# Performance work log

Hardware: AMD Instinct MI355X
Metric: run time of the kernel (lower is better)

## Reference

```python
import jax, jax.numpy as jnp
import numpy as np

BLK = 128          # quantization block size (group_shape = (1,128) act, (128,128) weight)
FP8_MAX = 448.0    # max finite value of float8_e4m3fn
EPS = 1e-6         # RMSNorm epsilon


def _rms_norm(x, weight):
    # RMSNorm: x / sqrt(mean(x^2) + eps) * weight
    var = jnp.mean(x * x, axis=-1, keepdims=True)
    return x * jax.lax.rsqrt(var + EPS) * weight


def _quant_dequant_act(x):
    # Per-token-group (1, BLK) dynamic FP8 quantization, then dequant (fake-quant).
    M, K = x.shape
    g = x.reshape(M, K // BLK, BLK)
    scale = jnp.maximum(jnp.max(jnp.abs(g), axis=-1, keepdims=True) / FP8_MAX, 1e-10)
    q = jnp.clip(g / scale, -FP8_MAX, FP8_MAX)
    q = q.astype(jnp.float8_e4m3fn).astype(jnp.float32)
    return (q * scale).reshape(M, K)


def _dequant_weight(w_fp8, ws):
    # w_fp8: [N, K] fp8-rounded values in fp32; ws: [N//BLK, K//BLK] block scales.
    s_full = jnp.repeat(jnp.repeat(ws, BLK, axis=0), BLK, axis=1)  # [N, K]
    return w_fp8 * s_full


def setup_inputs() -> dict:
    key = jax.random.key(0)
    k1, k2, k3, k4 = jax.random.split(key, 4)
    T, H = 4096, 4096
    x = jax.random.normal(k1, (T, H), dtype=jnp.float32)
    norm_w = jax.random.uniform(k2, (4, H), dtype=jnp.float32)
    w = jax.random.uniform(k3, (3, H, H), dtype=jnp.float32)
    wscale = jax.random.uniform(k4, (3, H // BLK, H // BLK), dtype=jnp.float32)
    return {"x": x, "norm_w": norm_w, "w": w, "wscale": wscale}


def reference(x, norm_w, w, wscale):
    # Weights are stored as FP8 in the original model (torch.rand(...).to(FP8_DTYPE)).
    w_fp8 = w.astype(jnp.float8_e4m3fn).astype(jnp.float32)  # [3, H, H]

    x = jax.nn.relu(x)
    resid = x
    # norm[0]: plain RMSNorm
    y = _rms_norm(x, norm_w[0])
    for i in range(3):
        # block-FP8 linear: quantize activation, dequantize weight, out = a @ W^T
        a = _quant_dequant_act(y)                    # [T, H]
        wd = _dequant_weight(w_fp8[i], wscale[i])    # [H, H]
        xi = a @ wd.T                                # [T, H]
        # fused add + RMSNorm: resid = xi + resid; y = rmsnorm(resid)
        resid = xi + resid
        y = _rms_norm(resid, norm_w[i + 1])
    return y
```

## Files before the change

### kernel.cpp

```cpp
#include <hip/hip_runtime.h>

typedef float f32x4 __attribute__((ext_vector_type(4)));
typedef long lx2 __attribute__((ext_vector_type(2)));

#define HDIM 4096
#define NKB 32

__device__ __forceinline__ int frag_off(int off) {
  const int o = off & 127;
  return (off & ~127) + (o & 64) + ((o & 24) << 1) + ((o & 32) >> 2) + (o & 7);
}

__global__ __launch_bounds__(256) void wquant_kernel(const float* __restrict__ w,
                                                     unsigned char* __restrict__ w8,
                                                     int n4) {
  int i = blockIdx.x * 256 + threadIdx.x;
  if (i >= n4) return;
  const float4 v = ((const float4*)w)[i];
  int p = 0;
  p = __builtin_amdgcn_cvt_pk_fp8_f32(v.x, v.y, p, false);
  p = __builtin_amdgcn_cvt_pk_fp8_f32(v.z, v.w, p, true);
  const int row = i >> 10;
  const int off = (i << 2) & 4095;
  *(int*)(w8 + (size_t)row * HDIM + frag_off(off)) = p;
}

template <int MODE>
__global__ __launch_bounds__(256) void norm_quant_kernel(
    const float* __restrict__ src, float* __restrict__ resid,
    const float* __restrict__ nw, unsigned char* __restrict__ qa,
    float* __restrict__ ascT, float* __restrict__ out) {
  const int row = blockIdx.x;
  const int tid = threadIdx.x;
  const float* srow = src + (size_t)row * HDIM;
  float4 v[4];
  float ss = 0.f;
#pragma unroll
  for (int c = 0; c < 4; ++c) {
    float4 t = ((const float4*)srow)[c * 256 + tid];
    if (MODE == 0) {
      t.x = fmaxf(t.x, 0.f); t.y = fmaxf(t.y, 0.f);
      t.z = fmaxf(t.z, 0.f); t.w = fmaxf(t.w, 0.f);
      ((float4*)(resid + (size_t)row * HDIM))[c * 256 + tid] = t;
    }
    v[c] = t;
    ss += t.x * t.x + t.y * t.y + t.z * t.z + t.w * t.w;
  }
#pragma unroll
  for (int m = 32; m >= 1; m >>= 1) ss += __shfl_xor(ss, m);
  __shared__ float red[4];
  if ((tid & 63) == 0) red[tid >> 6] = ss;
  __syncthreads();
  const float tot = red[0] + red[1] + red[2] + red[3];
  const float rstd = rsqrtf(tot * (1.f / (float)HDIM) + 1e-6f);
#pragma unroll
  for (int c = 0; c < 4; ++c) {
    float4 wv = ((const float4*)nw)[c * 256 + tid];
    float4 y;
    y.x = v[c].x * rstd * wv.x;
    y.y = v[c].y * rstd * wv.y;
    y.z = v[c].z * rstd * wv.z;
    y.w = v[c].w * rstd * wv.w;
    if (MODE == 2) {
      ((float4*)(out + (size_t)row * HDIM))[c * 256 + tid] = y;
    } else {
      float amax = fmaxf(fmaxf(fabsf(y.x), fabsf(y.y)), fmaxf(fabsf(y.z), fabsf(y.w)));
#pragma unroll
      for (int m = 16; m >= 1; m >>= 1) amax = fmaxf(amax, __shfl_xor(amax, m));
      const float scale = fmaxf(amax / 448.f, 1e-10f);
      const float qinv = __builtin_amdgcn_rcpf(scale);
      float qx = fminf(fmaxf(y.x * qinv, -448.f), 448.f);
      float qy = fminf(fmaxf(y.y * qinv, -448.f), 448.f);
      float qz = fminf(fmaxf(y.z * qinv, -448.f), 448.f);
      float qw = fminf(fmaxf(y.w * qinv, -448.f), 448.f);
      int p = 0;
      p = __builtin_amdgcn_cvt_pk_fp8_f32(qx, qy, p, false);
      p = __builtin_amdgcn_cvt_pk_fp8_f32(qz, qw, p, true);
      const int off = (c * 256 + tid) << 2;
      *(int*)(qa + (size_t)row * HDIM + frag_off(off)) = p;
      if ((tid & 31) == 0) ascT[(c * 8 + (tid >> 5)) * HDIM + row] = scale;
    }
  }
}

__device__ __forceinline__ f32x4 chain4(const lx2 (&a)[2], const lx2 (&b)[2]) {
  f32x4 t = __builtin_amdgcn_mfma_f32_16x16x32_fp8_fp8(a[0].x, b[0].x,
                                                       (f32x4){0.f, 0.f, 0.f, 0.f}, 0, 0, 0);
  t = __builtin_amdgcn_mfma_f32_16x16x32_fp8_fp8(a[0].y, b[0].y, t, 0, 0, 0);
  t = __builtin_amdgcn_mfma_f32_16x16x32_fp8_fp8(a[1].x, b[1].x, t, 0, 0, 0);
  t = __builtin_amdgcn_mfma_f32_16x16x32_fp8_fp8(a[1].y, b[1].y, t, 0, 0, 0);
  return t;
}

__global__ __launch_bounds__(512, 2) void gemm256_kernel(
    const unsigned char* __restrict__ qa, const float* __restrict__ ascT,
    const unsigned char* __restrict__ w8, const float* __restrict__ wsc,
    float* __restrict__ resid) {
  extern __shared__ char smem[];
  char* ldsA = smem;
  char* ldsB = smem + 65536;
  char* ldsS = smem + 131072;

  const int tid = threadIdx.x;
  const int lane = tid & 63;
  const int wid = tid >> 6;
  const int wm = wid >> 1;
  const int wn = wid & 1;

  const int bflat = blockIdx.y * 16 + blockIdx.x;
  const int bswz = (bflat & 7) * 32 + (bflat >> 3);
  const int m0 = (bswz >> 4) << 8;
  const int n0 = (bswz & 15) << 8;

  const int ln15 = lane & 15;
  const int g = lane >> 4;

  int ofsA[4], ofsB[4];
  {
    const int mt_ = (tid >> 7) & 3, kh_ = (tid >> 6) & 1;
    const int col = kh_ * 64 + ((tid >> 4) & 3) * 16;
    const int rr_ = tid & 15;
#pragma unroll
    for (int ch = 0; ch < 4; ++ch) {
      ofsA[ch] = (ch * 64 + mt_ * 16 + rr_) * HDIM + col;
      ofsB[ch] = ((ch >> 1) * 128 + ((ch & 1) * 4 + mt_) * 16 + rr_) * HDIM + col;
    }
  }
  const unsigned char* gA = qa + (size_t)m0 * HDIM;
  const unsigned char* gB = w8 + (size_t)n0 * HDIM;
  const float* sS = ascT + m0 + lane * 4;

  const int nb = __builtin_amdgcn_readfirstlane((n0 >> 7) + wn);
  const float* wsp = wsc + nb * NKB;

  const int abase = wm * 8192 + lane * 16;
  const int bbase = wn * 16384 + lane * 16;
  const int svb = wm * 256 + g * 16;

  f32x4 acc[4][8];
#pragma unroll
  for (int i = 0; i < 4; ++i)
#pragma unroll
    for (int j = 0; j < 8; ++j) acc[i][j] = (f32x4){0.f, 0.f, 0.f, 0.f};

  lx2 aF[4][2];
  lx2 bFa[2][2];
  lx2 bFb[2][2];
  f32x4 svw[4];

#define STAGE_A(CH, KB, BUF)                                                              \
  __builtin_amdgcn_global_load_lds(                                                       \
      (const __attribute__((address_space(1))) void*)(gA + ofsA[CH] + (KB)*128),          \
      (__attribute__((address_space(3))) void*)(ldsA + (BUF)*32768 + (CH)*8192 + tid*16), \
      16, 0, 0)
#define STAGE_B(CH, KB, BUF)                                                              \
  __builtin_amdgcn_global_load_lds(                                                       \
      (const __attribute__((address_space(1))) void*)(gB + ofsB[CH] + (KB)*128),          \
      (__attribute__((address_space(3))) void*)(ldsB + (BUF)*32768 + (CH)*8192 + tid*16), \
      16, 0, 0)
#define STAGE_S(KB, BUF)                                                                  \
  __builtin_amdgcn_global_load_lds(                                                       \
      (const __attribute__((address_space(1))) void*)(sS + (size_t)(KB)*HDIM),            \
      (__attribute__((address_space(3))) void*)(ldsS + (BUF)*1024 + lane*16), 16, 0, 0)

#define RD_A(MT)                                                                          \
  aF[MT][0] = *(const lx2*)(ldsA + cb + abase + (MT)*2048);                               \
  aF[MT][1] = *(const lx2*)(ldsA + cb + abase + (MT)*2048 + 1024);
#define RD_SVW(MT) svw[MT] = *(const f32x4*)(ldsS + cur * 1024 + svb + (MT)*64) * sw;
#define RD_BS(BS, NH)                                                                     \
  BS[0][0] = *(const lx2*)(ldsB + cb + bbase + ((NH)*2) * 2048);                          \
  BS[0][1] = *(const lx2*)(ldsB + cb + bbase + ((NH)*2) * 2048 + 1024);                   \
  BS[1][0] = *(const lx2*)(ldsB + cb + bbase + ((NH)*2 + 1) * 2048);                      \
  BS[1][1] = *(const lx2*)(ldsB + cb + bbase + ((NH)*2 + 1) * 2048 + 1024);

#define PH_SYNC                                                                           \
  __builtin_amdgcn_s_barrier();                                                           \
  asm volatile("s_waitcnt lgkmcnt(0)" ::: "memory");                                      \
  __builtin_amdgcn_sched_barrier(0);

#define MFMA_PH(MTA, MTB, NH, BS)                                                         \
  __builtin_amdgcn_s_setprio(1);                                                          \
  {                                                                                       \
    f32x4 t0 = chain4(aF[MTA], BS[0]);                                                    \
    f32x4 t1 = chain4(aF[MTA], BS[1]);                                                    \
    f32x4 t2 = chain4(aF[MTB], BS[0]);                                                    \
    f32x4 t3 = chain4(aF[MTB], BS[1]);                                                    \
    __builtin_amdgcn_s_setprio(0);                                                        \
    acc[MTA][(NH)*2]     += t0 * svw[MTA];                                                \
    acc[MTA][(NH)*2 + 1] += t1 * svw[MTA];                                                \
    acc[MTB][(NH)*2]     += t2 * svw[MTB];                                                \
    acc[MTB][(NH)*2 + 1] += t3 * svw[MTB];                                                \
  }

  STAGE_S(0, 0); STAGE_A(0, 0, 0); STAGE_A(1, 0, 0); STAGE_A(2, 0, 0); STAGE_A(3, 0, 0);
  STAGE_B(0, 0, 0); STAGE_B(2, 0, 0); STAGE_B(1, 0, 0); STAGE_B(3, 0, 0);
  asm volatile("s_waitcnt vmcnt(2)" ::: "memory");
  __builtin_amdgcn_s_barrier();

#pragma unroll 2
  for (int kb = 0; kb < NKB; ++kb) {
    const int cur = kb & 1;
    const int nxt = cur ^ 1;
    const int kbn = (kb + 1) & (NKB - 1);
    const int cb = cur * 32768;
    const float sw = wsp[kb];
    RD_A(0) RD_A(1) RD_SVW(0) RD_SVW(1) RD_BS(bFa, 0)
    STAGE_S(kbn, nxt); STAGE_A(0, kbn, nxt);
    PH_SYNC MFMA_PH(0, 1, 0, bFa)
    __builtin_amdgcn_s_barrier();
    RD_A(2) RD_A(3) RD_SVW(2) RD_SVW(3)
    STAGE_A(1, kbn, nxt); STAGE_A(2, kbn, nxt);
    PH_SYNC MFMA_PH(2, 3, 0, bFa)
    __builtin_amdgcn_s_barrier();
    RD_BS(bFb, 1)
    STAGE_A(3, kbn, nxt); STAGE_B(0, kbn, nxt);
    PH_SYNC MFMA_PH(2, 3, 1, bFb)
    __builtin_amdgcn_s_barrier();
    PH_SYNC MFMA_PH(0, 1, 1, bFb)
    asm volatile("s_waitcnt vmcnt(6)" ::: "memory");
    __builtin_amdgcn_s_barrier();
    RD_BS(bFa, 2)
    STAGE_B(2, kbn, nxt);
    PH_SYNC MFMA_PH(0, 1, 2, bFa)
    __builtin_amdgcn_s_barrier();
    STAGE_B(1, kbn, nxt);
    PH_SYNC MFMA_PH(2, 3, 2, bFa)
    __builtin_amdgcn_s_barrier();
    RD_BS(bFb, 3)
    STAGE_B(3, kbn, nxt);
    PH_SYNC MFMA_PH(2, 3, 3, bFb)
    __builtin_amdgcn_s_barrier();
    PH_SYNC MFMA_PH(0, 1, 3, bFb)
    asm volatile("s_waitcnt vmcnt(2)" ::: "memory");
    __builtin_amdgcn_s_barrier();
  }

  const size_t rowstart = (size_t)(m0 + wm * 64 + g * 4) * HDIM + n0 + wn * 128 + ln15;
#pragma unroll
  for (int mt = 0; mt < 4; ++mt)
#pragma unroll
    for (int ntg = 0; ntg < 8; ++ntg)
#pragma unroll
      for (int j = 0; j < 4; ++j) {
        const size_t idx = rowstart + (size_t)(mt * 16 + j) * HDIM + ntg * 16;
        resid[idx] += acc[mt][ntg][j];
      }
#undef MFMA_PH
#undef PH_SYNC
#undef RD_BS
#undef RD_SVW
#undef RD_A
#undef STAGE_A
#undef STAGE_B
#undef STAGE_S
}

extern "C" void kernel_launch(void* const* d_in, const int* in_sizes, int n_in,
                              void* d_out, int out_size, void* d_ws, size_t ws_size,
                              hipStream_t stream) {
  const float* x = (const float*)d_in[0];
  const float* norm_w = (const float*)d_in[1];
  const float* w = (const float*)d_in[2];
  const float* wscale = (const float*)d_in[3];
  float* out = (float*)d_out;
  char* ws = (char*)d_ws;

  size_t off = 0;
  unsigned char* w8 = (unsigned char*)(ws + off); off += 3ull * HDIM * HDIM;
  float* resid = (float*)(ws + off);              off += (size_t)HDIM * HDIM * 4;
  unsigned char* qa = (unsigned char*)(ws + off); off += (size_t)HDIM * HDIM;
  float* asc = (float*)(ws + off);                off += (size_t)NKB * HDIM * 4;

  hipFuncSetAttribute((const void*)gemm256_kernel,
                      hipFuncAttributeMaxDynamicSharedMemorySize, 133120);

  const int n4 = 3 * HDIM * HDIM / 4;
  wquant_kernel<<<n4 / 256, 256, 0, stream>>>(w, w8, n4);
  norm_quant_kernel<0><<<HDIM, 256, 0, stream>>>(x, resid, norm_w, qa, asc, nullptr);
  for (int i = 0; i < 3; ++i) {
    gemm256_kernel<<<dim3(16, 16), 512, 133120, stream>>>(
        qa, asc, w8 + (size_t)i * HDIM * HDIM, wscale + i * NKB * NKB, resid);
    if (i < 2)
      norm_quant_kernel<1><<<HDIM, 256, 0, stream>>>(resid, nullptr, norm_w + (size_t)(i + 1) * HDIM, qa, asc, nullptr);
    else
      norm_quant_kernel<2><<<HDIM, 256, 0, stream>>>(resid, nullptr, norm_w + (size_t)3 * HDIM, nullptr, nullptr, out);
  }
}
```

Measured before the change: 478.6 us.

## Use 16x16x128 scaled FP8 MFMA and drop fragment-permuted layouts

Replaces each chain of four 16x16x32 FP8 MFMAs with a single gfx950 mfma_scale 16x16x128 f8f6f4 instruction using a neutral scale of 127. Because that instruction takes contiguous 32-byte K fragments, the quantization kernels now store FP8 activations and weights in plain row-major order instead of a permuted fragment layout, and the GEMM staging offsets are unified. The aim is fewer, denser matrix instructions and simpler quant stores. The risk is that the new K-ordering in LDS must match the operand layout the wider instruction expects, otherwise results would be wrong.

```diff
diff --git a/kernel.cpp b/kernel.cpp
--- a/kernel.cpp
+++ b/kernel.cpp
@@ -1,15 +1,11 @@
 #include <hip/hip_runtime.h>
 
 typedef float f32x4 __attribute__((ext_vector_type(4)));
-typedef long lx2 __attribute__((ext_vector_type(2)));
+typedef int i32x4 __attribute__((ext_vector_type(4)));
+typedef int i32x8 __attribute__((ext_vector_type(8)));
 
 #define HDIM 4096
 #define NKB 32
-
-__device__ __forceinline__ int frag_off(int off) {
-  const int o = off & 127;
-  return (off & ~127) + (o & 64) + ((o & 24) << 1) + ((o & 32) >> 2) + (o & 7);
-}
 
 __global__ __launch_bounds__(256) void wquant_kernel(const float* __restrict__ w,
                                                      unsigned char* __restrict__ w8,
@@ -20,9 +16,7 @@
   int p = 0;
   p = __builtin_amdgcn_cvt_pk_fp8_f32(v.x, v.y, p, false);
   p = __builtin_amdgcn_cvt_pk_fp8_f32(v.z, v.w, p, true);
-  const int row = i >> 10;
-  const int off = (i << 2) & 4095;
-  *(int*)(w8 + (size_t)row * HDIM + frag_off(off)) = p;
+  ((int*)w8)[i] = p;
 }
 
 template <int MODE>
@@ -77,19 +71,10 @@
       p = __builtin_amdgcn_cvt_pk_fp8_f32(qx, qy, p, false);
       p = __builtin_amdgcn_cvt_pk_fp8_f32(qz, qw, p, true);
       const int off = (c * 256 + tid) << 2;
-      *(int*)(qa + (size_t)row * HDIM + frag_off(off)) = p;
+      *(int*)(qa + (size_t)row * HDIM + off) = p;
       if ((tid & 31) == 0) ascT[(c * 8 + (tid >> 5)) * HDIM + row] = scale;
     }
   }
-}
-
-__device__ __forceinline__ f32x4 chain4(const lx2 (&a)[2], const lx2 (&b)[2]) {
-  f32x4 t = __builtin_amdgcn_mfma_f32_16x16x32_fp8_fp8(a[0].x, b[0].x,
-                                                       (f32x4){0.f, 0.f, 0.f, 0.f}, 0, 0, 0);
-  t = __builtin_amdgcn_mfma_f32_16x16x32_fp8_fp8(a[0].y, b[0].y, t, 0, 0, 0);
-  t = __builtin_amdgcn_mfma_f32_16x16x32_fp8_fp8(a[1].x, b[1].x, t, 0, 0, 0);
-  t = __builtin_amdgcn_mfma_f32_16x16x32_fp8_fp8(a[1].y, b[1].y, t, 0, 0, 0);
-  return t;
 }
 
 __global__ __launch_bounds__(512, 2) void gemm256_kernel(
@@ -115,16 +100,12 @@
   const int ln15 = lane & 15;
   const int g = lane >> 4;
 
-  int ofsA[4], ofsB[4];
+  int ofs[4];
   {
-    const int mt_ = (tid >> 7) & 3, kh_ = (tid >> 6) & 1;
-    const int col = kh_ * 64 + ((tid >> 4) & 3) * 16;
-    const int rr_ = tid & 15;
-#pragma unroll
-    for (int ch = 0; ch < 4; ++ch) {
-      ofsA[ch] = (ch * 64 + mt_ * 16 + rr_) * HDIM + col;
-      ofsB[ch] = ((ch >> 1) * 128 + ((ch & 1) * 4 + mt_) * 16 + rr_) * HDIM + col;
-    }
+    const int rowp = ((tid >> 7) & 3) * 16 + (tid & 15);
+    const int kp = ((tid >> 4) & 3) * 32 + ((tid >> 6) & 1) * 16;
+#pragma unroll
+    for (int ch = 0; ch < 4; ++ch) ofs[ch] = (ch * 64 + rowp) * HDIM + kp;
   }
   const unsigned char* gA = qa + (size_t)m0 * HDIM;
   const unsigned char* gB = w8 + (size_t)n0 * HDIM;
@@ -143,19 +124,19 @@
 #pragma unroll
     for (int j = 0; j < 8; ++j) acc[i][j] = (f32x4){0.f, 0.f, 0.f, 0.f};
 
-  lx2 aF[4][2];
-  lx2 bFa[2][2];
-  lx2 bFb[2][2];
+  i32x8 aF[4];
+  i32x8 bFa[2];
+  i32x8 bFb[2];
   f32x4 svw[4];
 
 #define STAGE_A(CH, KB, BUF)                                                              \
   __builtin_amdgcn_global_load_lds(                                                       \
-      (const __attribute__((address_space(1))) void*)(gA + ofsA[CH] + (KB)*128),          \
+      (const __attribute__((address_space(1))) void*)(gA + ofs[CH] + (KB)*128),           \
       (__attribute__((address_space(3))) void*)(ldsA + (BUF)*32768 + (CH)*8192 + tid*16), \
       16, 0, 0)
 #define STAGE_B(CH, KB, BUF)                                                              \
   __builtin_amdgcn_global_load_lds(                                                       \
-      (const __attribute__((address_space(1))) void*)(gB + ofsB[CH] + (KB)*128),          \
+      (const __attribute__((address_space(1))) void*)(gB + ofs[CH] + (KB)*128),           \
       (__attribute__((address_space(3))) void*)(ldsB + (BUF)*32768 + (CH)*8192 + tid*16), \
       16, 0, 0)
 #define STAGE_S(KB, BUF)                                                                  \
@@ -164,14 +145,24 @@
       (__attribute__((address_space(3))) void*)(ldsS + (BUF)*1024 + lane*16), 16, 0, 0)
 
 #define RD_A(MT)                                                                          \
-  aF[MT][0] = *(const lx2*)(ldsA + cb + abase + (MT)*2048);                               \
-  aF[MT][1] = *(const lx2*)(ldsA + cb + abase + (MT)*2048 + 1024);
+  {                                                                                       \
+    const char* pA_ = ldsA + cb + abase + (MT)*2048;                                      \
+    i32x4 lo_ = *(const i32x4*)pA_;                                                       \
+    i32x4 hi_ = *(const i32x4*)(pA_ + 1024);                                              \
+    aF[MT] = __builtin_shufflevector(lo_, hi_, 0, 1, 2, 3, 4, 5, 6, 7);                   \
+  }
 #define RD_SVW(MT) svw[MT] = *(const f32x4*)(ldsS + cur * 1024 + svb + (MT)*64) * sw;
 #define RD_BS(BS, NH)                                                                     \
-  BS[0][0] = *(const lx2*)(ldsB + cb + bbase + ((NH)*2) * 2048);                          \
-  BS[0][1] = *(const lx2*)(ldsB + cb + bbase + ((NH)*2) * 2048 + 1024);                   \
-  BS[1][0] = *(const lx2*)(ldsB + cb + bbase + ((NH)*2 + 1) * 2048);                      \
-  BS[1][1] = *(const lx2*)(ldsB + cb + bbase + ((NH)*2 + 1) * 2048 + 1024);
+  {                                                                                       \
+    const char* p0_ = ldsB + cb + bbase + ((NH)*2) * 2048;                                \
+    i32x4 l0_ = *(const i32x4*)p0_;                                                       \
+    i32x4 h0_ = *(const i32x4*)(p0_ + 1024);                                              \
+    BS[0] = __builtin_shufflevector(l0_, h0_, 0, 1, 2, 3, 4, 5, 6, 7);                    \
+    const char* p1_ = p0_ + 2048;                                                         \
+    i32x4 l1_ = *(const i32x4*)p1_;                                                       \
+    i32x4 h1_ = *(const i32x4*)(p1_ + 1024);                                              \
+    BS[1] = __builtin_shufflevector(l1_, h1_, 0, 1, 2, 3, 4, 5, 6, 7);                    \
+  }
 
 #define PH_SYNC                                                                           \
   __builtin_amdgcn_s_barrier();                                                           \
@@ -181,10 +172,15 @@
 #define MFMA_PH(MTA, MTB, NH, BS)                                                         \
   __builtin_amdgcn_s_setprio(1);                                                          \
   {                                                                                       \
-    f32x4 t0 = chain4(aF[MTA], BS[0]);                                                    \
-    f32x4 t1 = chain4(aF[MTA], BS[1]);                                                    \
-    f32x4 t2 = chain4(aF[MTB], BS[0]);                                                    \
-    f32x4 t3 = chain4(aF[MTB], BS[1]);                                                    \
+    const f32x4 z_ = (f32x4){0.f, 0.f, 0.f, 0.f};                                         \
+    f32x4 t0 = __builtin_amdgcn_mfma_scale_f32_16x16x128_f8f6f4(                          \
+        aF[MTA], BS[0], z_, 0, 0, 0, 127, 0, 127);                                        \
+    f32x4 t1 = __builtin_amdgcn_mfma_scale_f32_16x16x128_f8f6f4(                          \
+        aF[MTA], BS[1], z_, 0, 0, 0, 127, 0, 127);                                        \
+    f32x4 t2 = __builtin_amdgcn_mfma_scale_f32_16x16x128_f8f6f4(                          \
+        aF[MTB], BS[0], z_, 0, 0, 0, 127, 0, 127);                                        \
+    f32x4 t3 = __builtin_amdgcn_mfma_scale_f32_16x16x128_f8f6f4(                          \
+        aF[MTB], BS[1], z_, 0, 0, 0, 127, 0, 127);                                        \
     __builtin_amdgcn_s_setprio(0);                                                        \
     acc[MTA][(NH)*2]     += t0 * svw[MTA];                                                \
     acc[MTA][(NH)*2 + 1] += t1 * svw[MTA];                                                \
```

After: 423.1 us. 1.13x faster.
